# Performance work log

Hardware: AMD Instinct MI355X
Metric: run time of the kernel (lower is better)

## Reference

```python
import jax, jax.numpy as jnp
import numpy as np

B, SQ, SKV, D = 4, 4096, 4096, 64

def setup_inputs() -> dict:
    key = jax.random.key(0)
    kq, kv = jax.random.split(key)
    query = jax.random.normal(kq, (B, SQ, D), dtype=jnp.float32)
    value = jax.random.normal(kv, (B, SKV, D), dtype=jnp.float32)
    return {"query": query, "value": value}

def reference(query, value):
    # scores = Q @ V^T  (value acts as both keys and values; no 1/sqrt(d) scaling)
    scores = jnp.einsum('bqd,bkd->bqk', query, value)  # [B, SQ, SKV]
    dist = jax.nn.softmax(scores, axis=-1)
    context = jnp.einsum('bqk,bkd->bqd', dist, value)  # [B, SQ, D]
    return context
```

## Files before the change

kernel.cpp:

```cpp
#include <hip/hip_runtime.h>


#define NB   4
#define SQ   4096
#define SKV  4096
#define DH   64
#define L2E  1.44269504088896340736f

typedef _Float16 half8 __attribute__((ext_vector_type(8)));
typedef _Float16 half4 __attribute__((ext_vector_type(4)));
typedef _Float16 half2v __attribute__((ext_vector_type(2)));
typedef float f32x4 __attribute__((ext_vector_type(4)));
typedef unsigned short u16;

#define MFMA16(a, b, c) __builtin_amdgcn_mfma_f32_16x16x16f16((a), (b), (c), 0, 0, 0)
#define MFMA32(a, b, c) __builtin_amdgcn_mfma_f32_16x16x32_f16((a), (b), (c), 0, 0, 0)

__device__ __forceinline__ u16 f2h(float f) {
  _Float16 h = (_Float16)f;
  return __builtin_bit_cast(u16, h);
}
__device__ __forceinline__ half2v pkrtz(float a, float b) {
  return __builtin_bit_cast(half2v, __builtin_amdgcn_cvt_pkrtz(a, b));
}

typedef __attribute__((address_space(1))) void gvoid;
typedef __attribute__((address_space(3))) void lvoid;
__device__ __forceinline__ void dma16(const u16* g, u16* l) {
  __builtin_amdgcn_global_load_lds((gvoid*)g, (lvoid*)l, 16, 0, 0);
}

__global__ __launch_bounds__(256) void prep_kernel(
    const float* __restrict__ V, u16* __restrict__ vh, u16* __restrict__ vt) {
  __shared__ u16 ldsT[16 * 72];
  int blk = blockIdx.x;
  int b   = blk >> 8;
  int rem = blk & 255;
  int j0  = (rem >> 2) << 6;
  int d0  = (rem & 3) << 4;
  int t   = threadIdx.x;
  int j   = t >> 2;
  int dc  = (t & 3) << 2;

  const float* src = V + ((size_t)(b * SKV) + j0 + j) * DH + d0 + dc;
  float4 v4 = *(const float4*)src;
  u16 h[4] = {f2h(v4.x), f2h(v4.y), f2h(v4.z), f2h(v4.w)};
  unsigned p0 = (unsigned)h[0] | ((unsigned)h[1] << 16);
  unsigned p1 = (unsigned)h[2] | ((unsigned)h[3] << 16);
  int dfull = d0 + dc;
  int physd = ((((dfull >> 3) ^ (j & 7)) << 3)) + (dfull & 7);
  *(uint2*)(vh + ((size_t)(b * SKV) + j0 + j) * DH + physd) = make_uint2(p0, p1);

#pragma unroll
  for (int k = 0; k < 4; ++k) ldsT[(dc + k) * 72 + j] = h[k];
  __syncthreads();

  int dl = t >> 4;
  int jc = (t & 15) << 2;
  u16 tr[4];
#pragma unroll
  for (int k = 0; k < 4; ++k) tr[k] = ldsT[dl * 72 + jc + k];
  unsigned q0 = (unsigned)tr[0] | ((unsigned)tr[1] << 16);
  unsigned q1 = (unsigned)tr[2] | ((unsigned)tr[3] << 16);
  int drow = d0 + dl;
  int physj = ((((jc >> 3) ^ (drow & 7)) << 3)) + (jc & 7);
  *(uint2*)(vt + ((size_t)(b * DH) + drow) * SKV + j0 + physj) = make_uint2(q0, q1);
}

__global__ __launch_bounds__(256, 3) void attn_kernel(
    const float* __restrict__ Q,
    const u16* __restrict__ vh,
    const u16* __restrict__ vt,
    u16* __restrict__ po,
    float* __restrict__ pm,
    float* __restrict__ pl,
    int S, int kvLen) {
  __shared__ __align__(16) u16 lds[2][2][64 * 64];

  int blk  = blockIdx.x;
  int tile = blk / S;
  int s    = blk - tile * S;
  int b    = tile >> 5;
  int q0   = (tile & 31) << 7;
  int kv0  = s * kvLen;
  int t    = threadIdx.x;
  int wave = t >> 6;
  int lane = t & 63;
  int col  = lane & 15;
  int quad = lane >> 4;
  int qw   = q0 + (wave << 5);
  int c7   = col & 7;

  const u16* gv  = vh + (size_t)(b * SKV) * DH;
  const u16* gvt = vt + (size_t)(b * DH) * SKV;

  int r0 = t >> 3;
  int c0 = (t & 7) << 3;
  int wb = wave << 9;

  half8 qf[2][2];
#pragma unroll
  for (int set = 0; set < 2; ++set) {
#pragma unroll
    for (int kc = 0; kc < 2; ++kc) {
      const float* qp = Q + ((size_t)(b * SQ) + qw + set * 16 + col) * DH +
                        kc * 32 + (quad << 3);
      float4 a0 = *(const float4*)qp;
      float4 a1 = *(const float4*)(qp + 4);
      half8 h;
      h[0] = (_Float16)(a0.x * L2E); h[1] = (_Float16)(a0.y * L2E);
      h[2] = (_Float16)(a0.z * L2E); h[3] = (_Float16)(a0.w * L2E);
      h[4] = (_Float16)(a1.x * L2E); h[5] = (_Float16)(a1.y * L2E);
      h[6] = (_Float16)(a1.z * L2E); h[7] = (_Float16)(a1.w * L2E);
      qf[set][kc] = h;
    }
  }

  f32x4 o[2][4];
  float m_r[2] = {-1e30f, -1e30f};
  float l_r[2] = {0.f, 0.f};
#pragma unroll
  for (int set = 0; set < 2; ++set)
#pragma unroll
    for (int nf = 0; nf < 4; ++nf) o[set][nf] = (f32x4){0.f, 0.f, 0.f, 0.f};

  {
    u16* dv  = (u16*)&lds[0][0][0];
    u16* dvt = (u16*)&lds[0][1][0];
    dma16(gv + ((size_t)(kv0 + r0) << 6) + c0,        dv + wb);
    dma16(gv + ((size_t)(kv0 + r0 + 32) << 6) + c0,   dv + 2048 + wb);
    dma16(gvt + (size_t)r0 * SKV + kv0 + c0,          dvt + wb);
    dma16(gvt + (size_t)(r0 + 32) * SKV + kv0 + c0,   dvt + 2048 + wb);
  }

  int nIter = kvLen >> 6;
  int cur = 0;
  for (int it = 0; it < nIter; ++it) {
    __syncthreads();

    if ((it + 1) < nIter) {
      int j0n = kv0 + ((it + 1) << 6);
      u16* dv  = (u16*)&lds[cur ^ 1][0][0];
      u16* dvt = (u16*)&lds[cur ^ 1][1][0];
      dma16(gv + ((size_t)(j0n + r0) << 6) + c0,       dv + wb);
      dma16(gv + ((size_t)(j0n + r0 + 32) << 6) + c0,  dv + 2048 + wb);
      dma16(gvt + (size_t)r0 * SKV + j0n + c0,         dvt + wb);
      dma16(gvt + (size_t)(r0 + 32) * SKV + j0n + c0,  dvt + 2048 + wb);
    }

    const u16* sv  = &lds[cur][0][0];
    const u16* svt = &lds[cur][1][0];

    f32x4 sf[2][4];
#pragma unroll
    for (int set = 0; set < 2; ++set)
#pragma unroll
      for (int nf = 0; nf < 4; ++nf) sf[set][nf] = (f32x4){0.f, 0.f, 0.f, 0.f};
#pragma unroll
    for (int nf = 0; nf < 4; ++nf) {
#pragma unroll
      for (int kc = 0; kc < 2; ++kc) {
        int ch = ((kc << 2) + quad) ^ c7;
        half8 av = *(const half8*)(sv + ((nf * 16 + col) << 6) + (ch << 3));
        sf[0][nf] = MFMA32(av, qf[0][kc], sf[0][nf]);
        sf[1][nf] = MFMA32(av, qf[1][kc], sf[1][nf]);
      }
    }

    half4 pf[2][4];
#pragma unroll
    for (int set = 0; set < 2; ++set) {
      float tm = sf[set][0][0];
#pragma unroll
      for (int nf = 0; nf < 4; ++nf)
#pragma unroll
        for (int r = 0; r < 4; ++r) tm = fmaxf(tm, sf[set][nf][r]);
      tm = fmaxf(tm, __shfl_xor(tm, 16, 64));
      tm = fmaxf(tm, __shfl_xor(tm, 32, 64));
      float mn = fmaxf(m_r[set], tm);
      float al = exp2f(m_r[set] - mn);
      m_r[set] = mn;
      float rs = 0.f;
#pragma unroll
      for (int nf = 0; nf < 4; ++nf) {
        float p0 = exp2f(sf[set][nf][0] - mn);
        float p1 = exp2f(sf[set][nf][1] - mn);
        float p2 = exp2f(sf[set][nf][2] - mn);
        float p3 = exp2f(sf[set][nf][3] - mn);
        rs += (p0 + p1) + (p2 + p3);
        half2v lo = pkrtz(p0, p1);
        half2v hi = pkrtz(p2, p3);
        pf[set][nf] = __builtin_shufflevector(lo, hi, 0, 1, 2, 3);
      }
      l_r[set] = l_r[set] * al + rs;
#pragma unroll
      for (int nf = 0; nf < 4; ++nf)
#pragma unroll
        for (int r = 0; r < 4; ++r) o[set][nf][r] *= al;
    }

#pragma unroll
    for (int kc4 = 0; kc4 < 4; ++kc4) {
#pragma unroll
      for (int nf2 = 0; nf2 < 4; ++nf2) {
        int ch = ((kc4 << 1) + (quad >> 1)) ^ c7;
        half4 avt = *(const half4*)(svt + ((nf2 * 16 + col) << 6) +
                                    (ch << 3) + ((quad & 1) << 2));
        o[0][nf2] = MFMA16(avt, pf[0][kc4], o[0][nf2]);
        o[1][nf2] = MFMA16(avt, pf[1][kc4], o[1][nf2]);
      }
    }

    cur ^= 1;
  }

#pragma unroll
  for (int set = 0; set < 2; ++set) {
    l_r[set] += __shfl_xor(l_r[set], 16, 64);
    l_r[set] += __shfl_xor(l_r[set], 32, 64);
  }
  int pidx = tile * S + s;
  if (quad == 0) {
#pragma unroll
    for (int set = 0; set < 2; ++set) {
      int row = (wave << 5) + set * 16 + col;
      pm[(size_t)pidx * 128 + row] = m_r[set];
      pl[(size_t)pidx * 128 + row] = l_r[set];
    }
  }

  __syncthreads();
  u16* tp = (u16*)&lds[0][0][0];
#pragma unroll
  for (int set = 0; set < 2; ++set) {
    int q = (wave << 5) + set * 16 + col;
#pragma unroll
    for (int nf2 = 0; nf2 < 4; ++nf2) {
#pragma unroll
      for (int r2 = 0; r2 < 4; r2 += 2) {
        unsigned pk = (unsigned)f2h(o[set][nf2][r2]) |
                      ((unsigned)f2h(o[set][nf2][r2 + 1]) << 16);
        int d = nf2 * 16 + (quad << 2) + r2;
        *(unsigned*)(tp + q * 72 + d) = pk;
      }
    }
  }
  __syncthreads();
  {
    u16* pob = po + (size_t)pidx * 128 * 64;
    int q = t >> 1, hc = (t & 1) << 5;
    uint4 x0 = *(const uint4*)(tp + q * 72 + hc);
    uint4 x1 = *(const uint4*)(tp + q * 72 + hc + 8);
    uint4 x2 = *(const uint4*)(tp + q * 72 + hc + 16);
    uint4 x3 = *(const uint4*)(tp + q * 72 + hc + 24);
    *(uint4*)(pob + q * 64 + hc)      = x0;
    *(uint4*)(pob + q * 64 + hc + 8)  = x1;
    *(uint4*)(pob + q * 64 + hc + 16) = x2;
    *(uint4*)(pob + q * 64 + hc + 24) = x3;
  }
}

__global__ __launch_bounds__(256) void combine_kernel(
    const u16* __restrict__ po,
    const float* __restrict__ pm,
    const float* __restrict__ pl,
    float* __restrict__ out, int S) {
  int t    = threadIdx.x;
  int rowg = blockIdx.x * 32 + (t >> 3);
  int tile = rowg >> 7;
  int row  = rowg & 127;
  int dc   = (t & 7) << 3;

  float mv[8], lv[8];
  float M = -1e30f;
  for (int s = 0; s < S; ++s) {
    mv[s] = pm[(size_t)(tile * S + s) * 128 + row];
    lv[s] = pl[(size_t)(tile * S + s) * 128 + row];
    M = fmaxf(M, mv[s]);
  }
  float L = 0.f, w[8];
  for (int s = 0; s < S; ++s) {
    w[s] = exp2f(mv[s] - M);
    L += lv[s] * w[s];
  }
  float acc[8] = {0.f, 0.f, 0.f, 0.f, 0.f, 0.f, 0.f, 0.f};
  for (int s = 0; s < S; ++s) {
    const u16* p = po + (size_t)(tile * S + s) * 8192 + row * 64 + dc;
    uint4 raw = *(const uint4*)p;
    half8 x = __builtin_bit_cast(half8, raw);
#pragma unroll
    for (int k = 0; k < 8; ++k) acc[k] += w[s] * (float)x[k];
  }
  float invL = 1.0f / L;
  float* op = out + (size_t)rowg * 64 + dc;
  f32x4 o0 = (f32x4){acc[0], acc[1], acc[2], acc[3]};
  f32x4 o1 = (f32x4){acc[4], acc[5], acc[6], acc[7]};
  *(f32x4*)op       = o0 * invL;
  *(f32x4*)(op + 4) = o1 * invL;
}

extern "C" void kernel_launch(void* const* d_in, const int* in_sizes, int n_in,
                              void* d_out, int out_size, void* d_ws, size_t ws_size,
                              hipStream_t stream) {
  const float* Q = (const float*)d_in[0];
  const float* V = (const float*)d_in[1];
  float* out = (float*)d_out;

  const size_t convBytes = (size_t)2 * NB * SKV * DH * 2;
  auto partBytes = [](int S) {
    return (size_t)NB * 32 * S * ((size_t)128 * 64 * 2 + 128 * 8);
  };
  int S = 8;
  while (S > 1 && ws_size < convBytes + partBytes(S)) S >>= 1;
  int kvLen = SKV / S;

  u16* vh = (u16*)d_ws;
  u16* vt = vh + (size_t)NB * SKV * DH;
  u16* po = vt + (size_t)NB * SKV * DH;
  float* pm = (float*)(po + (size_t)NB * 32 * S * 128 * 64);
  float* pl = pm + (size_t)NB * 32 * S * 128;

  prep_kernel<<<NB * 256, 256, 0, stream>>>(V, vh, vt);
  attn_kernel<<<NB * 32 * S, 256, 0, stream>>>(Q, vh, vt, po, pm, pl, S, kvLen);
  combine_kernel<<<NB * SQ / 32, 256, 0, stream>>>(po, pm, pl, out, S);
}
```

Baseline: 109.3 us.

## Give each wave private LDS buffers and drop block-wide barriers in attention loop

Each of the four waves now loads its own 32-key V and V^T tiles into a private double-buffered LDS region. It waits with s_waitcnt on its own DMAs instead of using __syncthreads, which removes cross-wave barrier stalls. The V^T swizzle moves from the prep kernel's global layout into the in-wave load pattern. The KV split count drops from 8 to 4 and the occupancy hint is removed. Each block now loads the same KV tiles four times, so LDS use and L2 traffic rise in exchange for barrier-free pipelining. The hand-coded waitcnt values are a correctness risk.

```diff
diff --git a/kernel.cpp b/kernel.cpp
--- a/kernel.cpp
+++ b/kernel.cpp
@@ -62,12 +62,10 @@
   for (int k = 0; k < 4; ++k) tr[k] = ldsT[dl * 72 + jc + k];
   unsigned q0 = (unsigned)tr[0] | ((unsigned)tr[1] << 16);
   unsigned q1 = (unsigned)tr[2] | ((unsigned)tr[3] << 16);
-  int drow = d0 + dl;
-  int physj = ((((jc >> 3) ^ (drow & 7)) << 3)) + (jc & 7);
-  *(uint2*)(vt + ((size_t)(b * DH) + drow) * SKV + j0 + physj) = make_uint2(q0, q1);
-}
-
-__global__ __launch_bounds__(256, 3) void attn_kernel(
+  *(uint2*)(vt + ((size_t)(b * DH) + d0 + dl) * SKV + j0 + jc) = make_uint2(q0, q1);
+}
+
+__global__ __launch_bounds__(256) void attn_kernel(
     const float* __restrict__ Q,
     const u16* __restrict__ vh,
     const u16* __restrict__ vt,
@@ -75,7 +73,7 @@
     float* __restrict__ pm,
     float* __restrict__ pl,
     int S, int kvLen) {
-  __shared__ __align__(16) u16 lds[2][2][64 * 64];
+  __shared__ __align__(16) u16 lds[4][2][2][2048];
 
   int blk  = blockIdx.x;
   int tile = blk / S;
@@ -89,14 +87,15 @@
   int col  = lane & 15;
   int quad = lane >> 4;
   int qw   = q0 + (wave << 5);
-  int c7   = col & 7;
 
   const u16* gv  = vh + (size_t)(b * SKV) * DH;
   const u16* gvt = vt + (size_t)(b * DH) * SKV;
 
-  int r0 = t >> 3;
-  int c0 = (t & 7) << 3;
-  int wb = wave << 9;
+  int r3 = lane >> 3;
+  int c8 = (lane & 7) << 3;
+  int r2 = lane >> 2;
+  int cl = lane & 3;
+  int csw = ((cl ^ (r2 & 3)) << 3);
 
   half8 qf[2][2];
 #pragma unroll
@@ -124,55 +123,62 @@
 #pragma unroll
     for (int nf = 0; nf < 4; ++nf) o[set][nf] = (f32x4){0.f, 0.f, 0.f, 0.f};
 
+  u16* wV[2]  = {&lds[0][0][0][0], &lds[0][1][0][0]};
+  wV[0] = &lds[wave][0][0][0];  wV[1] = &lds[wave][1][0][0];
+  u16* wT[2]; wT[0] = &lds[wave][0][1][0]; wT[1] = &lds[wave][1][1][0];
+
   {
-    u16* dv  = (u16*)&lds[0][0][0];
-    u16* dvt = (u16*)&lds[0][1][0];
-    dma16(gv + ((size_t)(kv0 + r0) << 6) + c0,        dv + wb);
-    dma16(gv + ((size_t)(kv0 + r0 + 32) << 6) + c0,   dv + 2048 + wb);
-    dma16(gvt + (size_t)r0 * SKV + kv0 + c0,          dvt + wb);
-    dma16(gvt + (size_t)(r0 + 32) * SKV + kv0 + c0,   dvt + 2048 + wb);
-  }
-
-  int nIter = kvLen >> 6;
+#pragma unroll
+    for (int i = 0; i < 4; ++i)
+      dma16(gv + ((size_t)(kv0 + i * 8 + r3) << 6) + c8, wV[0] + i * 512);
+#pragma unroll
+    for (int i = 0; i < 4; ++i)
+      dma16(gvt + (size_t)(i * 16 + r2) * SKV + kv0 + csw, wT[0] + i * 512);
+  }
+
+  int nIter = kvLen >> 5;
   int cur = 0;
   for (int it = 0; it < nIter; ++it) {
-    __syncthreads();
-
-    if ((it + 1) < nIter) {
-      int j0n = kv0 + ((it + 1) << 6);
-      u16* dv  = (u16*)&lds[cur ^ 1][0][0];
-      u16* dvt = (u16*)&lds[cur ^ 1][1][0];
-      dma16(gv + ((size_t)(j0n + r0) << 6) + c0,       dv + wb);
-      dma16(gv + ((size_t)(j0n + r0 + 32) << 6) + c0,  dv + 2048 + wb);
-      dma16(gvt + (size_t)r0 * SKV + j0n + c0,         dvt + wb);
-      dma16(gvt + (size_t)(r0 + 32) * SKV + j0n + c0,  dvt + 2048 + wb);
-    }
-
-    const u16* sv  = &lds[cur][0][0];
-    const u16* svt = &lds[cur][1][0];
-
-    f32x4 sf[2][4];
+    bool more = (it + 1) < nIter;
+    if (more) {
+      int j0n = kv0 + ((it + 1) << 5);
+#pragma unroll
+      for (int i = 0; i < 4; ++i)
+        dma16(gv + ((size_t)(j0n + i * 8 + r3) << 6) + c8, wV[cur ^ 1] + i * 512);
+#pragma unroll
+      for (int i = 0; i < 4; ++i)
+        dma16(gvt + (size_t)(i * 16 + r2) * SKV + j0n + csw, wT[cur ^ 1] + i * 512);
+      __builtin_amdgcn_s_waitcnt(0x0F78);
+    } else {
+      __builtin_amdgcn_s_waitcnt(0x0F70);
+    }
+    __builtin_amdgcn_sched_barrier(0);
+
+    const u16* sv = wV[cur];
+    const u16* st = wT[cur];
+
+    f32x4 sf[2][2];
 #pragma unroll
     for (int set = 0; set < 2; ++set)
 #pragma unroll
-      for (int nf = 0; nf < 4; ++nf) sf[set][nf] = (f32x4){0.f, 0.f, 0.f, 0.f};
-#pragma unroll
-    for (int nf = 0; nf < 4; ++nf) {
+      for (int nf = 0; nf < 2; ++nf) sf[set][nf] = (f32x4){0.f, 0.f, 0.f, 0.f};
+#pragma unroll
+    for (int nf = 0; nf < 2; ++nf) {
 #pragma unroll
       for (int kc = 0; kc < 2; ++kc) {
-        int ch = ((kc << 2) + quad) ^ c7;
+        int ch = ((kc << 2) + quad) ^ (col & 7);
         half8 av = *(const half8*)(sv + ((nf * 16 + col) << 6) + (ch << 3));
         sf[0][nf] = MFMA32(av, qf[0][kc], sf[0][nf]);
         sf[1][nf] = MFMA32(av, qf[1][kc], sf[1][nf]);
       }
     }
 
-    half4 pf[2][4];
+    half4 pf[2][2];
 #pragma unroll
     for (int set = 0; set < 2; ++set) {
       float tm = sf[set][0][0];
 #pragma unroll
-      for (int nf = 0; nf < 4; ++nf)
+      for (int nf = 0; nf < 2; ++nf)
 #pragma unroll
         for (int r = 0; r < 4; ++r) tm = fmaxf(tm, sf[set][nf][r]);
       tm = fmaxf(tm, __shfl_xor(tm, 16, 64));
@@ -182,7 +188,7 @@
       m_r[set] = mn;
       float rs = 0.f;
 #pragma unroll
-      for (int nf = 0; nf < 4; ++nf) {
+      for (int nf = 0; nf < 2; ++nf) {
         float p0 = exp2f(sf[set][nf][0] - mn);
         float p1 = exp2f(sf[set][nf][1] - mn);
         float p2 = exp2f(sf[set][nf][2] - mn);
@@ -200,12 +206,12 @@
     }
 
 #pragma unroll
-    for (int kc4 = 0; kc4 < 4; ++kc4) {
+    for (int kc4 = 0; kc4 < 2; ++kc4) {
 #pragma unroll
       for (int nf2 = 0; nf2 < 4; ++nf2) {
-        int ch = ((kc4 << 1) + (quad >> 1)) ^ c7;
-        half4 avt = *(const half4*)(svt + ((nf2 * 16 + col) << 6) +
-                                    (ch << 3) + ((quad & 1) << 2));
+        int p = ((kc4 << 1) + (quad >> 1)) ^ (col & 3);
+        half4 avt = *(const half4*)(st + ((nf2 * 16 + col) << 5) +
+                                    (p << 3) + ((quad & 1) << 2));
         o[0][nf2] = MFMA16(avt, pf[0][kc4], o[0][nf2]);
         o[1][nf2] = MFMA16(avt, pf[1][kc4], o[1][nf2]);
       }
@@ -229,11 +235,10 @@
     }
   }
 
-  __syncthreads();
-  u16* tp = (u16*)&lds[0][0][0];
+  u16* tp = &lds[wave][0][0][0];
 #pragma unroll
   for (int set = 0; set < 2; ++set) {
-    int q = (wave << 5) + set * 16 + col;
+    int ql = set * 16 + col;
 #pragma unroll
     for (int nf2 = 0; nf2 < 4; ++nf2) {
 #pragma unroll
@@ -241,22 +246,22 @@
         unsigned pk = (unsigned)f2h(o[set][nf2][r2]) |
                       ((unsigned)f2h(o[set][nf2][r2 + 1]) << 16);
         int d = nf2 * 16 + (quad << 2) + r2;
-        *(unsigned*)(tp + q * 72 + d) = pk;
+        *(unsigned*)(tp + ql * 72 + d) = pk;
       }
     }
   }
-  __syncthreads();
+  __builtin_amdgcn_sched_barrier(0);
   {
-    u16* pob = po + (size_t)pidx * 128 * 64;
-    int q = t >> 1, hc = (t & 1) << 5;
-    uint4 x0 = *(const uint4*)(tp + q * 72 + hc);
-    uint4 x1 = *(const uint4*)(tp + q * 72 + hc + 8);
-    uint4 x2 = *(const uint4*)(tp + q * 72 + hc + 16);
-    uint4 x3 = *(const uint4*)(tp + q * 72 + hc + 24);
-    *(uint4*)(pob + q * 64 + hc)      = x0;
-    *(uint4*)(pob + q * 64 + hc + 8)  = x1;
-    *(uint4*)(pob + q * 64 + hc + 16) = x2;
-    *(uint4*)(pob + q * 64 + hc + 24) = x3;
+    u16* pob = po + (size_t)pidx * 128 * 64 + ((size_t)wave << 5) * 64;
+    int ql = lane >> 1, hc = (lane & 1) << 5;
+    uint4 x0 = *(const uint4*)(tp + ql * 72 + hc);
+    uint4 x1 = *(const uint4*)(tp + ql * 72 + hc + 8);
+    uint4 x2 = *(const uint4*)(tp + ql * 72 + hc + 16);
+    uint4 x3 = *(const uint4*)(tp + ql * 72 + hc + 24);
+    *(uint4*)(pob + ql * 64 + hc)      = x0;
+    *(uint4*)(pob + ql * 64 + hc + 8)  = x1;
+    *(uint4*)(pob + ql * 64 + hc + 16) = x2;
+    *(uint4*)(pob + ql * 64 + hc + 24) = x3;
   }
 }
 
@@ -310,7 +315,7 @@
   auto partBytes = [](int S) {
     return (size_t)NB * 32 * S * ((size_t)128 * 64 * 2 + 128 * 8);
   };
-  int S = 8;
+  int S = 4;
   while (S > 1 && ws_size < convBytes + partBytes(S)) S >>= 1;
   int kvLen = SKV / S;
 
```

Result: slower. 125.6 us (+14.9%).
